# Performance work log

Hardware: AMD Instinct MI355X
Metric: run time of the kernel (lower is better)

The kernel has to match this reference:

```python
import jax, jax.numpy as jnp
import numpy as np

N = 8192
K = 16  # k neighbors; layer uses k+1 columns

def setup_inputs() -> dict:
    key = jax.random.key(0)
    k1, k2 = jax.random.split(key)
    data_input = jax.random.normal(k1, (N, N), dtype=jnp.float32)
    neighbor_indices = jax.random.randint(k2, (N, K + 1), 0, N, dtype=jnp.int64)
    return {"data_input": data_input, "neighbor_indices": neighbor_indices}

def reference(data_input, neighbor_indices):
    # Original builds a sparse (n,n) adjacency with ones at (i, Idx[i,j]),
    # multiplies elementwise with dense data_input, then row-sums.
    # Equivalent (including duplicate-index accumulation) to gathering each
    # row's k+1 neighbor scores and summing them.
    idx = neighbor_indices[:, : K + 1]                 # (n, k+1)
    gathered = jnp.take_along_axis(data_input, idx, axis=1)  # (n, k+1)
    A_raw = jnp.sum(gathered, axis=1)                  # (n,)
    alpha = jax.nn.softmax(A_raw)                      # (n,)
    return (alpha, A_raw)
```

## Files before the change

### kernel.cpp

```cpp
#include <hip/hip_runtime.h>
#include <math.h>

#define NROWS 8192
#define KP1 17

__global__ __launch_bounds__(256) void gather_sum_kernel(
    const float* __restrict__ data,
    const int* __restrict__ nidx,
    float* __restrict__ a_raw)
{
    int tid   = blockIdx.x * blockDim.x + threadIdx.x;
    int row   = tid >> 5;
    int lane  = tid & 31;
    if (row >= NROWS) return;

    float v = 0.0f;
    if (lane < KP1) {
        int c = nidx[row * KP1 + lane];
        v = data[(size_t)row * NROWS + (size_t)c];
    }
    #pragma unroll
    for (int off = 16; off > 0; off >>= 1)
        v += __shfl_down(v, off, 32);

    if (lane == 0) a_raw[row] = v;
}

__global__ __launch_bounds__(1024) void softmax_kernel(
    const float* __restrict__ a_raw,
    float* __restrict__ alpha)
{
    __shared__ float red[16];
    const int t    = threadIdx.x;
    const int wave = t >> 6;
    const int lane = t & 63;

    float vals[8];
    float m = -INFINITY;
    #pragma unroll
    for (int i = 0; i < 8; ++i) {
        vals[i] = a_raw[t + i * 1024];
        m = fmaxf(m, vals[i]);
    }
    #pragma unroll
    for (int off = 32; off > 0; off >>= 1)
        m = fmaxf(m, __shfl_down(m, off, 64));
    if (lane == 0) red[wave] = m;
    __syncthreads();
    if (wave == 0) {
        float mm = (lane < 16) ? red[lane] : -INFINITY;
        #pragma unroll
        for (int off = 8; off > 0; off >>= 1)
            mm = fmaxf(mm, __shfl_down(mm, off, 64));
        if (lane == 0) red[0] = mm;
    }
    __syncthreads();
    m = red[0];
    __syncthreads();

    float s = 0.0f;
    #pragma unroll
    for (int i = 0; i < 8; ++i) {
        vals[i] = expf(vals[i] - m);
        s += vals[i];
    }
    #pragma unroll
    for (int off = 32; off > 0; off >>= 1)
        s += __shfl_down(s, off, 64);
    if (lane == 0) red[wave] = s;
    __syncthreads();
    if (wave == 0) {
        float ss = (lane < 16) ? red[lane] : 0.0f;
        #pragma unroll
        for (int off = 8; off > 0; off >>= 1)
            ss += __shfl_down(ss, off, 64);
        if (lane == 0) red[0] = ss;
    }
    __syncthreads();
    const float inv = 1.0f / red[0];
    #pragma unroll
    for (int i = 0; i < 8; ++i)
        alpha[t + i * 1024] = vals[i] * inv;
}

extern "C" void kernel_launch(void* const* d_in, const int* in_sizes, int n_in,
                              void* d_out, int out_size, void* d_ws, size_t ws_size,
                              hipStream_t stream) {
    const float* data = (const float*)d_in[0];
    const int*   nidx = (const int*)d_in[1];
    float* alpha = (float*)d_out;
    float* a_raw = (float*)d_out + NROWS;

    gather_sum_kernel<<<(NROWS * 32) / 256, 256, 0, stream>>>(data, nidx, a_raw);
    softmax_kernel<<<1, 1024, 0, stream>>>(a_raw, alpha);
}
```

Measured before the change: 13.10 us.

## Fuse gather-sum and softmax into one kernel using a last-block reduction

Merges the gather/row-sum kernel and the single-block softmax into one launch. Each block computes exp of its row sums, writes a per-block partial sum, and increments an atomic counter; the last block to arrive reduces the partials and normalizes all rows with float4 stores. The max subtraction is dropped, which risks overflow for large inputs, and a memset of the counter is added before the kernel.

```diff
diff --git a/kernel.cpp b/kernel.cpp
--- a/kernel.cpp
+++ b/kernel.cpp
@@ -1,18 +1,29 @@
 #include <hip/hip_runtime.h>
 #include <math.h>
 
-#define NROWS 8192
-#define KP1 17
+#define NROWS   8192
+#define KP1     17
+#define ROWS_PER_BLOCK 8
+#define NBLOCKS (NROWS / ROWS_PER_BLOCK)
 
-__global__ __launch_bounds__(256) void gather_sum_kernel(
+
+__global__ __launch_bounds__(256) void fused_gather_softmax(
     const float* __restrict__ data,
-    const int* __restrict__ nidx,
-    float* __restrict__ a_raw)
+    const int*   __restrict__ nidx,
+    float*       __restrict__ alpha,
+    float*       __restrict__ a_raw,
+    float*       __restrict__ expv,
+    float*       __restrict__ partial,
+    unsigned int* __restrict__ counter)
 {
-    int tid   = blockIdx.x * blockDim.x + threadIdx.x;
-    int row   = tid >> 5;
-    int lane  = tid & 31;
-    if (row >= NROWS) return;
+    __shared__ float lds_exp[ROWS_PER_BLOCK];
+    __shared__ float red[4];
+    __shared__ int   lastf;
+
+    const int t        = threadIdx.x;
+    const int rowLocal = t >> 5;
+    const int lane     = t & 31;
+    const int row      = blockIdx.x * ROWS_PER_BLOCK + rowLocal;
 
     float v = 0.0f;
     if (lane < KP1) {
@@ -23,64 +34,49 @@
     for (int off = 16; off > 0; off >>= 1)
         v += __shfl_down(v, off, 32);
 
-    if (lane == 0) a_raw[row] = v;
-}
-
-__global__ __launch_bounds__(1024) void softmax_kernel(
-    const float* __restrict__ a_raw,
-    float* __restrict__ alpha)
-{
-    __shared__ float red[16];
-    const int t    = threadIdx.x;
-    const int wave = t >> 6;
-    const int lane = t & 63;
-
-    float vals[8];
-    float m = -INFINITY;
-    #pragma unroll
-    for (int i = 0; i < 8; ++i) {
-        vals[i] = a_raw[t + i * 1024];
-        m = fmaxf(m, vals[i]);
-    }
-    #pragma unroll
-    for (int off = 32; off > 0; off >>= 1)
-        m = fmaxf(m, __shfl_down(m, off, 64));
-    if (lane == 0) red[wave] = m;
-    __syncthreads();
-    if (wave == 0) {
-        float mm = (lane < 16) ? red[lane] : -INFINITY;
-        #pragma unroll
-        for (int off = 8; off > 0; off >>= 1)
-            mm = fmaxf(mm, __shfl_down(mm, off, 64));
-        if (lane == 0) red[0] = mm;
+    if (lane == 0) {
+        a_raw[row] = v;
+        float ev = expf(v);
+        expv[row] = ev;
+        lds_exp[rowLocal] = ev;
     }
     __syncthreads();
-    m = red[0];
+
+    if (t == 0) {
+        float s = 0.0f;
+        #pragma unroll
+        for (int i = 0; i < ROWS_PER_BLOCK; ++i) s += lds_exp[i];
+        partial[blockIdx.x] = s;
+        __threadfence();
+        unsigned int old = atomicAdd(counter, 1u);
+        lastf = (old == NBLOCKS - 1) ? 1 : 0;
+    }
     __syncthreads();
+    if (!lastf) return;
+
+    __threadfence();
 
     float s = 0.0f;
     #pragma unroll
-    for (int i = 0; i < 8; ++i) {
-        vals[i] = expf(vals[i] - m);
-        s += vals[i];
-    }
+    for (int i = 0; i < 4; ++i)
+        s += partial[t + i * 256];
     #pragma unroll
     for (int off = 32; off > 0; off >>= 1)
         s += __shfl_down(s, off, 64);
-    if (lane == 0) red[wave] = s;
+    if ((t & 63) == 0) red[t >> 6] = s;
     __syncthreads();
-    if (wave == 0) {
-        float ss = (lane < 16) ? red[lane] : 0.0f;
-        #pragma unroll
-        for (int off = 8; off > 0; off >>= 1)
-            ss += __shfl_down(ss, off, 64);
-        if (lane == 0) red[0] = ss;
-    }
+    if (t == 0) red[0] = (red[0] + red[1]) + (red[2] + red[3]);
     __syncthreads();
     const float inv = 1.0f / red[0];
+
+    const float4* e4 = (const float4*)expv;
+    float4*       a4 = (float4*)alpha;
     #pragma unroll
-    for (int i = 0; i < 8; ++i)
-        alpha[t + i * 1024] = vals[i] * inv;
+    for (int i = t; i < NROWS / 4; i += 256) {
+        float4 x = e4[i];
+        x.x *= inv; x.y *= inv; x.z *= inv; x.w *= inv;
+        a4[i] = x;
+    }
 }
 
 extern "C" void kernel_launch(void* const* d_in, const int* in_sizes, int n_in,
@@ -91,6 +87,11 @@
     float* alpha = (float*)d_out;
     float* a_raw = (float*)d_out + NROWS;
 
-    gather_sum_kernel<<<(NROWS * 32) / 256, 256, 0, stream>>>(data, nidx, a_raw);
-    softmax_kernel<<<1, 1024, 0, stream>>>(a_raw, alpha);
+    unsigned int* counter = (unsigned int*)d_ws;
+    float* expv    = (float*)((char*)d_ws + 256);
+    float* partial = (float*)((char*)d_ws + 256 + NROWS * sizeof(float));
+
+    hipMemsetAsync(counter, 0, sizeof(unsigned int), stream);
+    fused_gather_softmax<<<NBLOCKS, 256, 0, stream>>>(
+        data, nidx, alpha, a_raw, expv, partial, counter);
 }
```

After: 38.34 us. 193% more time.
